# Optimization experiments

Hardware: AMD Instinct MI355X
Metric: run time of the kernel (lower is better)

The kernel has to match this reference:

```python
import jax, jax.numpy as jnp
import numpy as np

EMBED_DIM = 1024
NUM_HEADS = 16
HEAD_DIM = EMBED_DIM // NUM_HEADS
BOARD = 32
SEQ = BOARD * BOARD
BATCH = 16


def setup_inputs() -> dict:
    key = jax.random.key(0)
    ks = jax.random.split(key, 6)
    x = jax.random.normal(ks[0], (BATCH, SEQ, EMBED_DIM), dtype=jnp.float32)
    scale = 1.0 / np.sqrt(EMBED_DIM)
    Wq = jax.random.normal(ks[1], (EMBED_DIM, EMBED_DIM), dtype=jnp.float32) * scale
    Wk = jax.random.normal(ks[2], (EMBED_DIM, EMBED_DIM), dtype=jnp.float32) * scale
    Wv = jax.random.normal(ks[3], (EMBED_DIM, EMBED_DIM), dtype=jnp.float32) * scale
    Wo = jax.random.normal(ks[4], (EMBED_DIM, EMBED_DIM), dtype=jnp.float32) * scale
    rel_bias = jax.random.normal(ks[5], (NUM_HEADS, 2 * BOARD - 1), dtype=jnp.float32)
    return {"x": x, "Wq": Wq, "Wk": Wk, "Wv": Wv, "Wo": Wo, "rel_bias": rel_bias}


def _rel_indices():
    # coords of the flattened H*W grid
    idx = jnp.arange(SEQ)
    rows = idx // BOARD
    cols = idx % BOARD
    offset = BOARD - 1
    rel_x = cols[None, :] - cols[:, None] + offset  # [S, S]
    rel_y = rows[None, :] - rows[:, None] + offset  # [S, S]
    return rel_x, rel_y


def reference(x, Wq, Wk, Wv, Wo, rel_bias):
    B, S, E = x.shape
    H, D = NUM_HEADS, HEAD_DIM
    # projections (Linear with bias=False: x @ W.T; weights here stored as [E, E] applied as x @ W)
    q = (x @ Wq).reshape(B, S, H, D).transpose(0, 2, 1, 3)  # [B,H,S,D]
    k = (x @ Wk).reshape(B, S, H, D).transpose(0, 2, 1, 3)
    v = (x @ Wv).reshape(B, S, H, D).transpose(0, 2, 1, 3)
    scores = jnp.einsum('bhqd,bhkd->bhqk', q, k) / jnp.sqrt(jnp.float32(D))
    rel_x, rel_y = _rel_indices()
    bias = rel_bias[:, rel_x] + rel_bias[:, rel_y]  # [H, S, S]
    scores = scores + bias[None]
    attn = jax.nn.softmax(scores, axis=-1)
    out = jnp.einsum('bhqk,bhkd->bhqd', attn, v)
    out = out.transpose(0, 2, 1, 3).reshape(B, S, E)
    return out @ Wo
```

## Files before the change

kernel.cpp:

```cpp
#include <hip/hip_runtime.h>

#define SEQ   1024
#define EMBED 1024
#define NH    16
#define HD    64
#define NB    16

typedef float facc4 __attribute__((ext_vector_type(4)));
typedef float facc16 __attribute__((ext_vector_type(16)));
typedef short frag8 __attribute__((ext_vector_type(8)));
typedef short sv4 __attribute__((ext_vector_type(4)));

__device__ __forceinline__ unsigned short f2bf(float f) {
  union { float f; unsigned int u; } c; c.f = f;
  unsigned int u = c.u;
  u += 0x7FFFu + ((u >> 16) & 1u);
  return (unsigned short)(u >> 16);
}

__device__ __forceinline__ unsigned int pk_bf16(float lo, float hi) {
  unsigned int r;
  asm("v_cvt_pk_bf16_f32 %0, %1, %2" : "=v"(r) : "v"(lo), "v"(hi));
  return r;
}

__device__ __forceinline__ void gl_lds16(const void* g, void* l) {
  __builtin_amdgcn_global_load_lds(
      (const __attribute__((address_space(1))) unsigned int*)g,
      (__attribute__((address_space(3))) unsigned int*)l, 16, 0, 0);
}

__global__ __launch_bounds__(256) void convert_x_kernel(
    const float* __restrict__ x, unsigned short* __restrict__ xb, int n8) {
  int stride = gridDim.x * blockDim.x;
  for (int i = blockIdx.x * blockDim.x + threadIdx.x; i < n8; i += stride) {
    const float4* src = (const float4*)(x + (size_t)i * 8);
    float4 v0 = src[0], v1 = src[1];
    frag8 o;
    o[0] = f2bf(v0.x); o[1] = f2bf(v0.y); o[2] = f2bf(v0.z); o[3] = f2bf(v0.w);
    o[4] = f2bf(v1.x); o[5] = f2bf(v1.y); o[6] = f2bf(v1.z); o[7] = f2bf(v1.w);
    *(frag8*)(xb + (size_t)i * 8) = o;
  }
}

__global__ __launch_bounds__(256) void transpose_w_kernel(
    const float* W0, const float* W1, const float* W2, const float* W3,
    unsigned short* T0, unsigned short* T1, unsigned short* T2, unsigned short* T3) {
  __shared__ float tw[64][65];
  const float* W; unsigned short* T;
  switch (blockIdx.z) {
    case 0: W = W0; T = T0; break;
    case 1: W = W1; T = T1; break;
    case 2: W = W2; T = T2; break;
    default: W = W3; T = T3; break;
  }
  int k0 = blockIdx.y * 64, n0 = blockIdx.x * 64;
  int t = threadIdx.x;
#pragma unroll
  for (int rep = 0; rep < 4; ++rep) {
    int c = rep * 256 + t;
    int row = c >> 4, ch = c & 15;
    float4 v = *(const float4*)(W + (size_t)(k0 + row) * 1024 + n0 + ch * 4);
    tw[row][ch * 4 + 0] = v.x; tw[row][ch * 4 + 1] = v.y;
    tw[row][ch * 4 + 2] = v.z; tw[row][ch * 4 + 3] = v.w;
  }
  __syncthreads();
#pragma unroll
  for (int rep = 0; rep < 2; ++rep) {
    int c = rep * 256 + t;
    int nrow = c >> 3, ch = c & 7;
    frag8 o;
#pragma unroll
    for (int i = 0; i < 8; ++i) o[i] = (short)f2bf(tw[ch * 8 + i][nrow]);
    *(frag8*)(T + (size_t)(n0 + nrow) * 1024 + k0 + ch * 8) = o;
  }
}

template <int MODE>
__global__ __launch_bounds__(512, 2) void gemm256(
    const unsigned short* __restrict__ A, const unsigned short* __restrict__ Bt,
    unsigned short* __restrict__ qo, unsigned short* __restrict__ ko,
    unsigned short* __restrict__ vto, float* __restrict__ fo, int N) {
  __shared__ unsigned short a_s[2][256 * 64];
  __shared__ unsigned short b_s[2][256 * 64];
  const int tid = threadIdx.x;
  const int w = tid >> 6, l = tid & 63;
  const int l15 = l & 15, l4 = l >> 4;
  const int wr = w >> 2, wc = w & 3;

  const int bid = blockIdx.x;
  const int xcd = bid & 7, j = bid >> 3;
  const int mt = xcd * 8 + (j & 7), nt = j >> 3;
  const int m0 = mt << 8, n0 = nt << 8;

  const int ldrow = l >> 3;
  const int swz8 = ((l & 7) ^ (ldrow & 7)) << 3;
  const unsigned short* Ab = A + (size_t)m0 * 1024;
  const unsigned short* Bb = Bt + (size_t)n0 * 1024;

  facc4 acc[8][4];
#pragma unroll
  for (int mi = 0; mi < 8; ++mi)
#pragma unroll
    for (int nj = 0; nj < 4; ++nj)
#pragma unroll
      for (int r = 0; r < 4; ++r) acc[mi][nj][r] = 0.f;

  auto STAGE = [&](int buf, int kt) {
#pragma unroll
    for (int i = 0; i < 4; ++i) {
      const int c = (w << 2) + i;
      gl_lds16(Ab + (size_t)kt * 64 + (size_t)((c << 3) + ldrow) * 1024 + swz8,
               &a_s[buf][c << 9]);
      gl_lds16(Bb + (size_t)kt * 64 + (size_t)((c << 3) + ldrow) * 1024 + swz8,
               &b_s[buf][c << 9]);
    }
  };

  STAGE(0, 0);
  STAGE(1, 1);
  asm volatile("s_waitcnt vmcnt(8)" ::: "memory");
  __builtin_amdgcn_s_barrier();

  const int rowA = (wr << 7) + l15;
  const int rowB = (wc << 6) + l15;

  for (int t = 0; t < 16; ++t) {
    const int cur = t & 1;
    const unsigned short* ap = a_s[cur];
    const unsigned short* bp = b_s[cur];
    frag8 af[8], bf[4];

#pragma unroll
    for (int mi = 0; mi < 8; ++mi) {
      const int r = rowA + (mi << 4);
      af[mi] = *(const frag8*)(ap + (r << 6) + ((l4 ^ (r & 7)) << 3));
    }
#pragma unroll
    for (int nj = 0; nj < 4; ++nj) {
      const int r = rowB + (nj << 4);
      bf[nj] = *(const frag8*)(bp + (r << 6) + ((l4 ^ (r & 7)) << 3));
    }
    __builtin_amdgcn_s_setprio(1);
#pragma unroll
    for (int mi = 0; mi < 8; ++mi)
#pragma unroll
      for (int nj = 0; nj < 4; ++nj)
        acc[mi][nj] = __builtin_amdgcn_mfma_f32_16x16x32_bf16(
            af[mi], bf[nj], acc[mi][nj], 0, 0, 0);
    __builtin_amdgcn_s_setprio(0);

    frag8 ag[8], bg[4];
#pragma unroll
    for (int mi = 0; mi < 8; ++mi) {
      const int r = rowA + (mi << 4);
      ag[mi] = *(const frag8*)(ap + (r << 6) + (((4 + l4) ^ (r & 7)) << 3));
    }
#pragma unroll
    for (int nj = 0; nj < 4; ++nj) {
      const int r = rowB + (nj << 4);
      bg[nj] = *(const frag8*)(bp + (r << 6) + (((4 + l4) ^ (r & 7)) << 3));
    }
    asm volatile("s_waitcnt lgkmcnt(0)" ::: "memory");
    __builtin_amdgcn_s_barrier();
    if (t + 2 < 16) STAGE(cur, t + 2);

    __builtin_amdgcn_s_setprio(1);
#pragma unroll
    for (int mi = 0; mi < 8; ++mi)
#pragma unroll
      for (int nj = 0; nj < 4; ++nj)
        acc[mi][nj] = __builtin_amdgcn_mfma_f32_16x16x32_bf16(
            ag[mi], bg[nj], acc[mi][nj], 0, 0, 0);
    __builtin_amdgcn_s_setprio(0);

    if (t < 14)       asm volatile("s_waitcnt vmcnt(8)" ::: "memory");
    else if (t == 14) asm volatile("s_waitcnt vmcnt(0)" ::: "memory");
    if (t < 15) __builtin_amdgcn_s_barrier();
  }

  const int m_base = m0 + (wr << 7);
  if (MODE == 0) {
    const int bb16 = (m_base >> 10) << 4;
#pragma unroll
    for (int nj = 0; nj < 4; ++nj) {
      const int n = n0 + (wc << 6) + (nj << 4) + l15;
      const int proj = n >> 10, rem = n & 1023;
      const int h = rem >> 6, d = rem & 63;
      const size_t bh16 = ((size_t)(bb16 + h)) << 16;
      if (proj == 2) {
#pragma unroll
        for (int mi = 0; mi < 8; ++mi) {
          const int s0 = (m_base + (mi << 4) + (l4 << 2)) & 1023;
          sv4 pv;
#pragma unroll
          for (int rr = 0; rr < 4; ++rr) pv[rr] = (short)f2bf(acc[mi][nj][rr]);
          *(sv4*)(vto + bh16 + ((size_t)d << 10) + s0) = pv;
        }
      } else {
        unsigned short* dst = (proj == 0) ? qo : ko;
#pragma unroll
        for (int mi = 0; mi < 8; ++mi)
#pragma unroll
          for (int rr = 0; rr < 4; ++rr) {
            const int s = (m_base + (mi << 4) + (l4 << 2) + rr) & 1023;
            dst[bh16 + (size_t)s * 64 + d] = f2bf(acc[mi][nj][rr]);
          }
      }
    }
  } else {
#pragma unroll
    for (int nj = 0; nj < 4; ++nj) {
      const int n = n0 + (wc << 6) + (nj << 4) + l15;
#pragma unroll
      for (int mi = 0; mi < 8; ++mi)
#pragma unroll
        for (int rr = 0; rr < 4; ++rr) {
          const int m = m_base + (mi << 4) + (l4 << 2) + rr;
          fo[(size_t)m * N + n] = acc[mi][nj][rr];
        }
    }
  }
}

__global__ __launch_bounds__(256, 4) void attn_kernel(
    const unsigned short* __restrict__ q, const unsigned short* __restrict__ k,
    const unsigned short* __restrict__ vt, const float* __restrict__ rel_bias,
    unsigned short* __restrict__ ao) {
  __shared__ unsigned short smem[16384];
  __shared__ float rb_s[63];
  unsigned short* k_s = smem;
  unsigned short* v_s = smem + 8192;

  const int bid = blockIdx.x;
  const int xcd = bid & 7, jj = bid >> 3;
  const int bh = xcd * 32 + (jj >> 3), qt = jj & 7;
  const int b = bh >> 4, h = bh & 15;
  const int t = threadIdx.x, w = t >> 6, l = t & 63;
  const int l31 = l & 31, hi = l >> 5;

  if (t < 63) rb_s[t] = rel_bias[h * 63 + t] * 1.44269504f;

  const unsigned short* qg = q + (size_t)bh * (SEQ * 64);
  const unsigned short* kg = k + (size_t)bh * (SEQ * 64);
  const unsigned short* vg = vt + (size_t)bh * (64 * SEQ);

  const int q0 = qt * 128 + w * 32;
  const int qr = q0 >> 5;

  frag8 qf[4];
#pragma unroll
  for (int s = 0; s < 4; ++s)
    qf[s] = *(const frag8*)(qg + (size_t)(q0 + l31) * 64 + s * 16 + hi * 8);

  auto STAGE = [&](int buf, int kt) {
#pragma unroll
    for (int i = 0; i < 2; ++i) {
      const int c = i * 256 + t;
      const int row = c >> 3, ch = c & 7;
      const int sw = (ch ^ (row & 7)) << 3;
      const int base = ((i * 256 + w * 64) << 3) + buf * 4096;
      gl_lds16(kg + (size_t)(kt * 64 + row) * 64 + sw, k_s + base);
      gl_lds16(vg + (size_t)row * SEQ + kt * 64 + sw, v_s + base);
    }
  };
  STAGE(0, 0);

  asm volatile("s_waitcnt lgkmcnt(0)" ::: "memory");
  __builtin_amdgcn_s_barrier();

  float bx[16];
#pragma unroll
  for (int r = 0; r < 16; ++r) {
    const int kc = (r & 3) + 8 * (r >> 2) + 4 * hi;
    bx[r] = rb_s[kc - l31 + 31];
  }

  float m_run = -1e30f, lsum = 0.f;
  facc16 o0, o1;
#pragma unroll
  for (int i = 0; i < 16; ++i) { o0[i] = 0.f; o1[i] = 0.f; }

  const float C1 = 0.125f * 1.44269504f;

  for (int kt = 0; kt < 16; ++kt) {
    const int p = kt & 1;
    if (kt < 15) {
      STAGE(p ^ 1, kt + 1);
      asm volatile("s_waitcnt vmcnt(4)" ::: "memory");
    } else {
      asm volatile("s_waitcnt vmcnt(0)" ::: "memory");
    }
    __builtin_amdgcn_s_barrier();

    const char* kp = (const char*)(k_s + p * 4096);
    const char* vp = (const char*)(v_s + p * 4096);

    facc16 sa[2];
    __builtin_amdgcn_s_setprio(1);
#pragma unroll
    for (int st = 0; st < 2; ++st) {
      facc16 z;
#pragma unroll
      for (int i = 0; i < 16; ++i) z[i] = 0.f;
#pragma unroll
      for (int s = 0; s < 4; ++s) {
        const int row = st * 32 + l31;
        const int byte_off = row * 128 + (((s * 2 + hi) ^ (row & 7)) << 4);
        frag8 kf = *(const frag8*)(kp + byte_off);
        z = __builtin_amdgcn_mfma_f32_32x32x16_bf16(kf, qf[s], z, 0, 0, 0);
      }
      sa[st] = z;
    }
    __builtin_amdgcn_s_setprio(0);

    const float by0 = rb_s[kt * 2 + 0 - qr + 31];
    const float by1 = rb_s[kt * 2 + 1 - qr + 31];
    float sc0[16], sc1[16];
#pragma unroll
    for (int r = 0; r < 16; ++r) {
      sc0[r] = __builtin_fmaf(sa[0][r], C1, bx[r]);
      sc1[r] = __builtin_fmaf(sa[1][r], C1, bx[r]);
    }
    float m0 = sc0[0], m1 = sc1[0];
#pragma unroll
    for (int r = 1; r < 16; ++r) { m0 = fmaxf(m0, sc0[r]); m1 = fmaxf(m1, sc1[r]); }
    float tm = fmaxf(m0 + by0, m1 + by1);
    tm = fmaxf(tm, __shfl_xor(tm, 32));
    if (!__all(tm <= m_run + 8.f)) {
      const float mn = fmaxf(m_run, tm);
      const float corr = __builtin_amdgcn_exp2f(m_run - mn);
      lsum *= corr;
#pragma unroll
      for (int i = 0; i < 16; ++i) { o0[i] *= corr; o1[i] *= corr; }
      m_run = mn;
    }
    const float mb0 = m_run - by0, mb1 = m_run - by1;
    float p0[16], p1[16];
    float ps = 0.f;
#pragma unroll
    for (int r = 0; r < 16; ++r) {
      p0[r] = __builtin_amdgcn_exp2f(sc0[r] - mb0);
      p1[r] = __builtin_amdgcn_exp2f(sc1[r] - mb1);
      ps += p0[r] + p1[r];
    }
    ps += __shfl_xor(ps, 32);
    lsum += ps;

    unsigned int fw[4][4];
#pragma unroll
    for (int ks = 0; ks < 4; ++ks) {
      const float* pp = (ks < 2) ? p0 : p1;
      const int R0 = (ks & 1) * 8;
      const int R1 = R0 + 4;
      const unsigned int w00 = pk_bf16(pp[R0 + 0], pp[R0 + 1]);
      const unsigned int w01 = pk_bf16(pp[R0 + 2], pp[R0 + 3]);
      const unsigned int w10 = pk_bf16(pp[R1 + 0], pp[R1 + 1]);
      const unsigned int w11 = pk_bf16(pp[R1 + 2], pp[R1 + 3]);
      const unsigned int s0 = hi ? w00 : w10;
      const unsigned int s1 = hi ? w01 : w11;
      const unsigned int r0 = __shfl_xor((int)s0, 32);
      const unsigned int r1 = __shfl_xor((int)s1, 32);
      fw[ks][0] = hi ? r0 : w00;
      fw[ks][1] = hi ? r1 : w01;
      fw[ks][2] = hi ? w10 : r0;
      fw[ks][3] = hi ? w11 : r1;
    }

    __builtin_amdgcn_s_setprio(1);
#pragma unroll
    for (int ks = 0; ks < 4; ++ks) {
      frag8 pb;
      {
        union { unsigned int u[4]; frag8 f; } cv;
        cv.u[0] = fw[ks][0]; cv.u[1] = fw[ks][1];
        cv.u[2] = fw[ks][2]; cv.u[3] = fw[ks][3];
        pb = cv.f;
      }
      {
        const int row = l31;
        const int byte_off = row * 128 + (((ks * 2 + hi) ^ (row & 7)) << 4);
        frag8 vf = *(const frag8*)(vp + byte_off);
        o0 = __builtin_amdgcn_mfma_f32_32x32x16_bf16(vf, pb, o0, 0, 0, 0);
      }
      {
        const int row = 32 + l31;
        const int byte_off = row * 128 + (((ks * 2 + hi) ^ (row & 7)) << 4);
        frag8 vf = *(const frag8*)(vp + byte_off);
        o1 = __builtin_amdgcn_mfma_f32_32x32x16_bf16(vf, pb, o1, 0, 0, 0);
      }
    }
    __builtin_amdgcn_s_setprio(0);

    asm volatile("s_waitcnt lgkmcnt(0)" ::: "memory");
    __builtin_amdgcn_s_barrier();
  }

  const float inv = __builtin_amdgcn_rcpf(lsum);
  unsigned short (*os)[72] = (unsigned short (*)[72])(smem + w * (32 * 72));
#pragma unroll
  for (int dt = 0; dt < 2; ++dt) {
#pragma unroll
    for (int r = 0; r < 16; r += 2) {
      const int d = (r & 3) + 8 * (r >> 2) + 4 * hi + 32 * dt;
      const float e0 = (dt ? o1[r] : o0[r]) * inv;
      const float e1 = (dt ? o1[r + 1] : o0[r + 1]) * inv;
      *(unsigned int*)&os[l31][d] = pk_bf16(e0, e1);
    }
  }
  asm volatile("s_waitcnt lgkmcnt(0)" ::: "memory");
#pragma unroll
  for (int i = 0; i < 4; ++i) {
    const int c = i * 64 + l;
    const int qrow = c >> 3, ch = c & 7;
    frag8 ov = *(const frag8*)(&os[qrow][ch * 8]);
    *(frag8*)(ao + ((size_t)(b * SEQ + q0 + qrow) * EMBED + h * 64 + ch * 8)) = ov;
  }
}

extern "C" void kernel_launch(void* const* d_in, const int* in_sizes, int n_in,
                              void* d_out, int out_size, void* d_ws, size_t ws_size,
                              hipStream_t stream) {
  (void)in_sizes; (void)n_in; (void)out_size; (void)ws_size;
  const float* x  = (const float*)d_in[0];
  const float* Wq = (const float*)d_in[1];
  const float* Wk = (const float*)d_in[2];
  const float* Wv = (const float*)d_in[3];
  const float* Wo = (const float*)d_in[4];
  const float* rb = (const float*)d_in[5];
  float* out = (float*)d_out;

  unsigned short* xb  = (unsigned short*)d_ws;
  unsigned short* wtq = xb + 16777216;
  unsigned short* wtk = wtq + 1048576;
  unsigned short* wtv = wtk + 1048576;
  unsigned short* wto = wtv + 1048576;
  unsigned short* qb  = wto + 1048576;
  unsigned short* kb  = qb + 16777216;
  unsigned short* aob = kb + 16777216;
  unsigned short* vtb = aob + 16777216;

  convert_x_kernel<<<4096, 256, 0, stream>>>(x, xb, 16777216 / 8);
  transpose_w_kernel<<<dim3(16, 16, 4), 256, 0, stream>>>(
      Wq, Wk, Wv, Wo, wtq, wtk, wtv, wto);
  gemm256<0><<<768, 512, 0, stream>>>(
      xb, wtq, qb, kb, vtb, nullptr, 3072);
  attn_kernel<<<2048, 256, 0, stream>>>(qb, kb, vtb, rb, aob);
  gemm256<1><<<256, 512, 0, stream>>>(
      aob, wto, nullptr, nullptr, nullptr, out, 1024);
}
```

Baseline: 271.6 us.

## Process two 32-row query tiles per wave in attention to reuse K/V LDS loads

Each attention wave now handles 64 query rows as two independent 32-row groups with separate online-softmax state. K fragments are loaded from LDS once and shared by both groups, and V fragments feed two MFMAs each. The grid halves to 1024 blocks and launch bounds drop to 2 waves/SIMD. This cuts LDS traffic and global K/V staging per query, at the cost of roughly doubled register pressure, lower occupancy and fewer blocks to fill the CUs.

```diff
diff --git a/kernel.cpp b/kernel.cpp
--- a/kernel.cpp
+++ b/kernel.cpp
@@ -223,7 +223,7 @@
   }
 }
 
-__global__ __launch_bounds__(256, 4) void attn_kernel(
+__global__ __launch_bounds__(256, 2) void attn_kernel(
     const unsigned short* __restrict__ q, const unsigned short* __restrict__ k,
     const unsigned short* __restrict__ vt, const float* __restrict__ rel_bias,
     unsigned short* __restrict__ ao) {
@@ -234,7 +234,7 @@
 
   const int bid = blockIdx.x;
   const int xcd = bid & 7, jj = bid >> 3;
-  const int bh = xcd * 32 + (jj >> 3), qt = jj & 7;
+  const int bh = xcd * 32 + (jj >> 2), qt = jj & 3;
   const int b = bh >> 4, h = bh & 15;
   const int t = threadIdx.x, w = t >> 6, l = t & 63;
   const int l31 = l & 31, hi = l >> 5;
@@ -245,13 +245,16 @@
   const unsigned short* kg = k + (size_t)bh * (SEQ * 64);
   const unsigned short* vg = vt + (size_t)bh * (64 * SEQ);
 
-  const int q0 = qt * 128 + w * 32;
-  const int qr = q0 >> 5;
-
-  frag8 qf[4];
-#pragma unroll
-  for (int s = 0; s < 4; ++s)
-    qf[s] = *(const frag8*)(qg + (size_t)(q0 + l31) * 64 + s * 16 + hi * 8);
+  const int q0 = qt * 256 + w * 64;
+  const int qrA = q0 >> 5;
+  const int qrB = qrA + 1;
+
+  frag8 qfA[4], qfB[4];
+#pragma unroll
+  for (int s = 0; s < 4; ++s) {
+    qfA[s] = *(const frag8*)(qg + (size_t)(q0 + l31) * 64 + s * 16 + hi * 8);
+    qfB[s] = *(const frag8*)(qg + (size_t)(q0 + 32 + l31) * 64 + s * 16 + hi * 8);
+  }
 
   auto STAGE = [&](int buf, int kt) {
 #pragma unroll
@@ -276,10 +279,10 @@
     bx[r] = rb_s[kc - l31 + 31];
   }
 
-  float m_run = -1e30f, lsum = 0.f;
-  facc16 o0, o1;
-#pragma unroll
-  for (int i = 0; i < 16; ++i) { o0[i] = 0.f; o1[i] = 0.f; }
+  float m_runA = -1e30f, lsumA = 0.f, m_runB = -1e30f, lsumB = 0.f;
+  facc16 oA0, oA1, oB0, oB1;
+#pragma unroll
+  for (int i = 0; i < 16; ++i) { oA0[i] = 0.f; oA1[i] = 0.f; oB0[i] = 0.f; oB1[i] = 0.f; }
 
   const float C1 = 0.125f * 1.44269504f;
 
@@ -295,99 +298,126 @@
 
     const char* kp = (const char*)(k_s + p * 4096);
     const char* vp = (const char*)(v_s + p * 4096);
-
-    facc16 sa[2];
-    __builtin_amdgcn_s_setprio(1);
-#pragma unroll
-    for (int st = 0; st < 2; ++st) {
-      facc16 z;
-#pragma unroll
-      for (int i = 0; i < 16; ++i) z[i] = 0.f;
+    const int kt2 = kt * 2;
+
+    frag8 kf[8];
+#pragma unroll
+    for (int st = 0; st < 2; ++st)
 #pragma unroll
       for (int s = 0; s < 4; ++s) {
         const int row = st * 32 + l31;
-        const int byte_off = row * 128 + (((s * 2 + hi) ^ (row & 7)) << 4);
-        frag8 kf = *(const frag8*)(kp + byte_off);
-        z = __builtin_amdgcn_mfma_f32_32x32x16_bf16(kf, qf[s], z, 0, 0, 0);
-      }
-      sa[st] = z;
-    }
-    __builtin_amdgcn_s_setprio(0);
-
-    const float by0 = rb_s[kt * 2 + 0 - qr + 31];
-    const float by1 = rb_s[kt * 2 + 1 - qr + 31];
-    float sc0[16], sc1[16];
-#pragma unroll
-    for (int r = 0; r < 16; ++r) {
-      sc0[r] = __builtin_fmaf(sa[0][r], C1, bx[r]);
-      sc1[r] = __builtin_fmaf(sa[1][r], C1, bx[r]);
-    }
-    float m0 = sc0[0], m1 = sc1[0];
-#pragma unroll
-    for (int r = 1; r < 16; ++r) { m0 = fmaxf(m0, sc0[r]); m1 = fmaxf(m1, sc1[r]); }
-    float tm = fmaxf(m0 + by0, m1 + by1);
-    tm = fmaxf(tm, __shfl_xor(tm, 32));
-    if (!__all(tm <= m_run + 8.f)) {
-      const float mn = fmaxf(m_run, tm);
-      const float corr = __builtin_amdgcn_exp2f(m_run - mn);
-      lsum *= corr;
-#pragma unroll
-      for (int i = 0; i < 16; ++i) { o0[i] *= corr; o1[i] *= corr; }
-      m_run = mn;
-    }
-    const float mb0 = m_run - by0, mb1 = m_run - by1;
-    float p0[16], p1[16];
-    float ps = 0.f;
-#pragma unroll
-    for (int r = 0; r < 16; ++r) {
-      p0[r] = __builtin_amdgcn_exp2f(sc0[r] - mb0);
-      p1[r] = __builtin_amdgcn_exp2f(sc1[r] - mb1);
-      ps += p0[r] + p1[r];
-    }
-    ps += __shfl_xor(ps, 32);
-    lsum += ps;
-
-    unsigned int fw[4][4];
+        kf[st * 4 + s] = *(const frag8*)(kp + row * 128 + (((s * 2 + hi) ^ (row & 7)) << 4));
+      }
+
+    auto SOFTMAX_FW = [&](const facc16& z0, const facc16& z1, int qr_,
+                          float& m_run_, float& lsum_, facc16& oo0, facc16& oo1,
+                          unsigned int (&fw_)[4][4]) {
+      const float by0 = rb_s[kt2 + 0 - qr_ + 31];
+      const float by1 = rb_s[kt2 + 1 - qr_ + 31];
+      float sc0[16], sc1[16];
+#pragma unroll
+      for (int r = 0; r < 16; ++r) {
+        sc0[r] = __builtin_fmaf(z0[r], C1, bx[r]);
+        sc1[r] = __builtin_fmaf(z1[r], C1, bx[r]);
+      }
+      float m0 = sc0[0], m1 = sc1[0];
+#pragma unroll
+      for (int r = 1; r < 16; ++r) { m0 = fmaxf(m0, sc0[r]); m1 = fmaxf(m1, sc1[r]); }
+      float tm = fmaxf(m0 + by0, m1 + by1);
+      tm = fmaxf(tm, __shfl_xor(tm, 32));
+      if (!__all(tm <= m_run_ + 8.f)) {
+        const float mn = fmaxf(m_run_, tm);
+        const float corr = __builtin_amdgcn_exp2f(m_run_ - mn);
+        lsum_ *= corr;
+#pragma unroll
+        for (int i = 0; i < 16; ++i) { oo0[i] *= corr; oo1[i] *= corr; }
+        m_run_ = mn;
+      }
+      const float mb0 = m_run_ - by0, mb1 = m_run_ - by1;
+      float p0[16], p1[16];
+      float ps = 0.f;
+#pragma unroll
+      for (int r = 0; r < 16; ++r) {
+        p0[r] = __builtin_amdgcn_exp2f(sc0[r] - mb0);
+        p1[r] = __builtin_amdgcn_exp2f(sc1[r] - mb1);
+        ps += p0[r] + p1[r];
+      }
+      ps += __shfl_xor(ps, 32);
+      lsum_ += ps;
+#pragma unroll
+      for (int ks = 0; ks < 4; ++ks) {
+        const float* pp = (ks < 2) ? p0 : p1;
+        const int R0 = (ks & 1) * 8;
+        const int R1 = R0 + 4;
+        const unsigned int w00 = pk_bf16(pp[R0 + 0], pp[R0 + 1]);
+        const unsigned int w01 = pk_bf16(pp[R0 + 2], pp[R0 + 3]);
+        const unsigned int w10 = pk_bf16(pp[R1 + 0], pp[R1 + 1]);
+        const unsigned int w11 = pk_bf16(pp[R1 + 2], pp[R1 + 3]);
+        const unsigned int s0 = hi ? w00 : w10;
+        const unsigned int s1 = hi ? w01 : w11;
+        const unsigned int r0 = __shfl_xor((int)s0, 32);
+        const unsigned int r1 = __shfl_xor((int)s1, 32);
+        fw_[ks][0] = hi ? r0 : w00;
+        fw_[ks][1] = hi ? r1 : w01;
+        fw_[ks][2] = hi ? w10 : r0;
+        fw_[ks][3] = hi ? w11 : r1;
+      }
+    };
+
+    unsigned int fwA[4][4], fwB[4][4];
+
+    {
+      facc16 z0, z1;
+#pragma unroll
+      for (int i = 0; i < 16; ++i) { z0[i] = 0.f; z1[i] = 0.f; }
+      __builtin_amdgcn_s_setprio(1);
+#pragma unroll
+      for (int s = 0; s < 4; ++s) {
+        z0 = __builtin_amdgcn_mfma_f32_32x32x16_bf16(kf[s], qfA[s], z0, 0, 0, 0);
+        z1 = __builtin_amdgcn_mfma_f32_32x32x16_bf16(kf[4 + s], qfA[s], z1, 0, 0, 0);
+      }
+      __builtin_amdgcn_s_setprio(0);
+      SOFTMAX_FW(z0, z1, qrA, m_runA, lsumA, oA0, oA1, fwA);
+    }
+
+    {
+      facc16 z0, z1;
+#pragma unroll
+      for (int i = 0; i < 16; ++i) { z0[i] = 0.f; z1[i] = 0.f; }
+      __builtin_amdgcn_s_setprio(1);
+#pragma unroll
+      for (int s = 0; s < 4; ++s) {
+        z0 = __builtin_amdgcn_mfma_f32_32x32x16_bf16(kf[s], qfB[s], z0, 0, 0, 0);
+        z1 = __builtin_amdgcn_mfma_f32_32x32x16_bf16(kf[4 + s], qfB[s], z1, 0, 0, 0);
+      }
+      __builtin_amdgcn_s_setprio(0);
+      SOFTMAX_FW(z0, z1, qrB, m_runB, lsumB, oB0, oB1, fwB);
+    }
+
+    __builtin_amdgcn_s_setprio(1);
 #pragma unroll
     for (int ks = 0; ks < 4; ++ks) {
-      const float* pp = (ks < 2) ? p0 : p1;
-      const int R0 = (ks & 1) * 8;
-      const int R1 = R0 + 4;
-      const unsigned int w00 = pk_bf16(pp[R0 + 0], pp[R0 + 1]);
-      const unsigned int w01 = pk_bf16(pp[R0 + 2], pp[R0 + 3]);
-      const unsigned int w10 = pk_bf16(pp[R1 + 0], pp[R1 + 1]);
-      const unsigned int w11 = pk_bf16(pp[R1 + 2], pp[R1 + 3]);
-      const unsigned int s0 = hi ? w00 : w10;
-      const unsigned int s1 = hi ? w01 : w11;
-      const unsigned int r0 = __shfl_xor((int)s0, 32);
-      const unsigned int r1 = __shfl_xor((int)s1, 32);
-      fw[ks][0] = hi ? r0 : w00;
-      fw[ks][1] = hi ? r1 : w01;
-      fw[ks][2] = hi ? w10 : r0;
-      fw[ks][3] = hi ? w11 : r1;
-    }
-
-    __builtin_amdgcn_s_setprio(1);
-#pragma unroll
-    for (int ks = 0; ks < 4; ++ks) {
-      frag8 pb;
+      frag8 pbA, pbB;
       {
         union { unsigned int u[4]; frag8 f; } cv;
-        cv.u[0] = fw[ks][0]; cv.u[1] = fw[ks][1];
-        cv.u[2] = fw[ks][2]; cv.u[3] = fw[ks][3];
-        pb = cv.f;
+        cv.u[0] = fwA[ks][0]; cv.u[1] = fwA[ks][1];
+        cv.u[2] = fwA[ks][2]; cv.u[3] = fwA[ks][3];
+        pbA = cv.f;
+        cv.u[0] = fwB[ks][0]; cv.u[1] = fwB[ks][1];
+        cv.u[2] = fwB[ks][2]; cv.u[3] = fwB[ks][3];
+        pbB = cv.f;
       }
       {
         const int row = l31;
-        const int byte_off = row * 128 + (((ks * 2 + hi) ^ (row & 7)) << 4);
-        frag8 vf = *(const frag8*)(vp + byte_off);
-        o0 = __builtin_amdgcn_mfma_f32_32x32x16_bf16(vf, pb, o0, 0, 0, 0);
+        frag8 vf = *(const frag8*)(vp + row * 128 + (((ks * 2 + hi) ^ (row & 7)) << 4));
+        oA0 = __builtin_amdgcn_mfma_f32_32x32x16_bf16(vf, pbA, oA0, 0, 0, 0);
+        oB0 = __builtin_amdgcn_mfma_f32_32x32x16_bf16(vf, pbB, oB0, 0, 0, 0);
       }
       {
         const int row = 32 + l31;
-        const int byte_off = row * 128 + (((ks * 2 + hi) ^ (row & 7)) << 4);
-        frag8 vf = *(const frag8*)(vp + byte_off);
-        o1 = __builtin_amdgcn_mfma_f32_32x32x16_bf16(vf, pb, o1, 0, 0, 0);
+        frag8 vf = *(const frag8*)(vp + row * 128 + (((ks * 2 + hi) ^ (row & 7)) << 4));
+        oA1 = __builtin_amdgcn_mfma_f32_32x32x16_bf16(vf, pbA, oA1, 0, 0, 0);
+        oB1 = __builtin_amdgcn_mfma_f32_32x32x16_bf16(vf, pbB, oB1, 0, 0, 0);
       }
     }
     __builtin_amdgcn_s_setprio(0);
@@ -396,25 +426,29 @@
     __builtin_amdgcn_s_barrier();
   }
 
-  const float inv = __builtin_amdgcn_rcpf(lsum);
   unsigned short (*os)[72] = (unsigned short (*)[72])(smem + w * (32 * 72));
 #pragma unroll
-  for (int dt = 0; dt < 2; ++dt) {
-#pragma unroll
-    for (int r = 0; r < 16; r += 2) {
-      const int d = (r & 3) + 8 * (r >> 2) + 4 * hi + 32 * dt;
-      const float e0 = (dt ? o1[r] : o0[r]) * inv;
-      const float e1 = (dt ? o1[r + 1] : o0[r + 1]) * inv;
-      *(unsigned int*)&os[l31][d] = pk_bf16(e0, e1);
-    }
-  }
-  asm volatile("s_waitcnt lgkmcnt(0)" ::: "memory");
-#pragma unroll
-  for (int i = 0; i < 4; ++i) {
-    const int c = i * 64 + l;
-    const int qrow = c >> 3, ch = c & 7;
-    frag8 ov = *(const frag8*)(&os[qrow][ch * 8]);
-    *(frag8*)(ao + ((size_t)(b * SEQ + q0 + qrow) * EMBED + h * 64 + ch * 8)) = ov;
+  for (int g = 0; g < 2; ++g) {
+    const float inv = __builtin_amdgcn_rcpf(g ? lsumB : lsumA);
+#pragma unroll
+    for (int dt = 0; dt < 2; ++dt) {
+      const facc16& oo = g ? (dt ? oB1 : oB0) : (dt ? oA1 : oA0);
+#pragma unroll
+      for (int r = 0; r < 16; r += 2) {
+        const int d = (r & 3) + 8 * (r >> 2) + 4 * hi + 32 * dt;
+        *(unsigned int*)&os[l31][d] = pk_bf16(oo[r] * inv, oo[r + 1] * inv);
+      }
+    }
+    asm volatile("s_waitcnt lgkmcnt(0)" ::: "memory");
+    const int qb = q0 + g * 32;
+#pragma unroll
+    for (int i = 0; i < 4; ++i) {
+      const int c = i * 64 + l;
+      const int qrow = c >> 3, ch = c & 7;
+      frag8 ov = *(const frag8*)(&os[qrow][ch * 8]);
+      *(frag8*)(ao + ((size_t)(b * SEQ + qb + qrow) * EMBED + h * 64 + ch * 8)) = ov;
+    }
+    asm volatile("s_waitcnt lgkmcnt(0)" ::: "memory");
   }
 }
 
@@ -445,7 +479,7 @@
       Wq, Wk, Wv, Wo, wtq, wtk, wtv, wto);
   gemm256<0><<<768, 512, 0, stream>>>(
       xb, wtq, qb, kb, vtb, nullptr, 3072);
-  attn_kernel<<<2048, 256, 0, stream>>>(qb, kb, vtb, rb, aob);
+  attn_kernel<<<1024, 256, 0, stream>>>(qb, kb, vtb, rb, aob);
   gemm256<1><<<256, 512, 0, stream>>>(
       aob, wto, nullptr, nullptr, nullptr, out, 1024);
 }
```

Measured after the change: 286.4 us. 5.4% more time.
